# Performance work log

Measured on AMD Instinct MI355X. Metric: run time of the kernel, lower is better.

The kernel has to match this reference:

```python
import jax, jax.numpy as jnp
import numpy as np

T, B, E, H = 512, 64, 256, 256


def setup_inputs() -> dict:
    key = jax.random.key(0)
    ks = jax.random.split(key, 14)
    def p(k, shape, s=0.05):
        return jax.random.normal(k, shape, dtype=jnp.float32) * s
    return {
        "inputs": jax.random.normal(ks[0], (T, B, E), dtype=jnp.float32),
        # attention params (nn.Parameter torch.randn -> unit scale)
        "rot": jax.random.normal(ks[1], (E, E), dtype=jnp.float32),
        "ent": jax.random.normal(ks[2], (E, E), dtype=jnp.float32),
        # gate linears: stored as (in, out) so y = x @ W + b (same math as torch Linear)
        "Wf": p(ks[3], (E + H, H)), "bf": jnp.zeros((H,), jnp.float32),
        "Wi": p(ks[4], (E + H, H)), "bi": jnp.zeros((H,), jnp.float32),
        "Wu": p(ks[5], (E + H, H)), "bu": jnp.zeros((H,), jnp.float32),
        "Wo": p(ks[6], (E + H, H)), "bo": jnp.zeros((H,), jnp.float32),
        "Wc": p(ks[7], (E, H)),     "bc": jnp.zeros((H,), jnp.float32),
    }


def reference(inputs, rot, ent, Wf, bf, Wi, bi, Wu, bu, Wo, bo, Wc, bc):
    t, b, e = inputs.shape
    h = Wf.shape[1]
    # --- one-shot self-attention (ClassicalSelfAttention) ---
    inp = inputs.transpose(1, 0, 2)                       # [B,T,E]
    q = jnp.einsum('bte,ef->btf', inp, rot)
    k = jnp.einsum('bte,ef->btf', inp, ent)
    scores = jax.nn.softmax(jnp.einsum('btf,bsf->bts', q, k) / jnp.sqrt(jnp.float32(e)), axis=-1)
    context = jnp.einsum('bts,bse->bte', scores, inp).transpose(1, 0, 2)  # [T,B,E]
    # context projection is time-invariant -> precompute as one big GEMM
    ctx_proj = context @ Wc + bc                          # [T,B,H]
    # --- recurrent LSTM cell over time via scan ---
    def step(carry, xs):
        hx, cx = carry
        x, cp = xs
        combined = jnp.concatenate([x, hx + cp], axis=1)  # [B,E+H]
        f = jax.nn.sigmoid(combined @ Wf + bf)
        i = jax.nn.sigmoid(combined @ Wi + bi)
        g = jnp.tanh(combined @ Wu + bu)
        o = jax.nn.sigmoid(combined @ Wo + bo)
        cx = f * cx + i * g
        hx = o * jnp.tanh(cx)
        return (hx, cx), hx
    hx0 = jnp.zeros((b, h), inputs.dtype)
    cx0 = jnp.zeros((b, h), inputs.dtype)
    (hx, cx), outputs = jax.lax.scan(step, (hx0, cx0), (inputs, ctx_proj))
    return outputs, hx, cx
```

## Files before the change

kernel.cpp:

```cpp
#include <hip/hip_runtime.h>

#define T_ 512
#define B_ 64
#define E_ 256
#define H_ 256

typedef __attribute__((ext_vector_type(8))) short short8_t;
typedef __attribute__((ext_vector_type(4))) float floatx4;

__device__ __forceinline__ unsigned short f2bf(float f) {
  unsigned int u = __float_as_uint(f);
  u += 0x7FFFu + ((u >> 16) & 1u);
  return (unsigned short)(u >> 16);
}
__device__ __forceinline__ float bf2f(unsigned short s) {
  return __uint_as_float(((unsigned int)s) << 16);
}
__device__ __forceinline__ float fast_tanh(float x) {
  float e = __expf(-2.0f * x);
  return 2.0f / (1.0f + e) - 1.0f;
}

__global__ __launch_bounds__(256) void qk_kernel(
    const float* __restrict__ inp, const float* __restrict__ rot,
    const float* __restrict__ ent, float* __restrict__ qo, float* __restrict__ ko)
{
  __shared__ __align__(16) float As[16][136];
  __shared__ __align__(16) float B1[16][68];
  __shared__ __align__(16) float B2[16][68];
  const int tid = threadIdx.x;
  const int m0 = blockIdx.y * 128, n0 = blockIdx.x * 64;
  const int lk = tid & 15, lm = tid >> 4;
  const int ln = tid & 63, lkb = tid >> 6;
  const int tx = tid & 15, ty = tid >> 4;
  float acc1[8][4], acc2[8][4];
#pragma unroll
  for (int i = 0; i < 8; ++i)
#pragma unroll
    for (int j = 0; j < 4; ++j) { acc1[i][j] = 0.f; acc2[i][j] = 0.f; }

  for (int k0 = 0; k0 < 256; k0 += 16) {
    __syncthreads();
#pragma unroll
    for (int p = 0; p < 8; ++p) {
      int m = lm + p * 16;
      As[lk][m] = inp[(size_t)(m0 + m) * 256 + k0 + lk];
    }
#pragma unroll
    for (int p = 0; p < 4; ++p) {
      int kk = lkb + p * 4;
      B1[kk][ln] = rot[(size_t)(k0 + kk) * 256 + n0 + ln];
      B2[kk][ln] = ent[(size_t)(k0 + kk) * 256 + n0 + ln];
    }
    __syncthreads();
#pragma unroll
    for (int kk = 0; kk < 16; ++kk) {
      floatx4 a_lo = *(const floatx4*)&As[kk][ty * 8];
      floatx4 a_hi = *(const floatx4*)&As[kk][ty * 8 + 4];
      floatx4 b1v = *(const floatx4*)&B1[kk][tx * 4];
      floatx4 b2v = *(const floatx4*)&B2[kk][tx * 4];
#pragma unroll
      for (int i = 0; i < 4; ++i) {
        float alo = a_lo[i], ahi = a_hi[i];
#pragma unroll
        for (int j = 0; j < 4; ++j) {
          acc1[i][j]     += alo * b1v[j];
          acc1[i + 4][j] += ahi * b1v[j];
          acc2[i][j]     += alo * b2v[j];
          acc2[i + 4][j] += ahi * b2v[j];
        }
      }
    }
  }
#pragma unroll
  for (int i = 0; i < 8; ++i) {
    size_t row = (size_t)(m0 + ty * 8 + i);
    float4 v1 = make_float4(acc1[i][0], acc1[i][1], acc1[i][2], acc1[i][3]);
    float4 v2 = make_float4(acc2[i][0], acc2[i][1], acc2[i][2], acc2[i][3]);
    *(float4*)&qo[row * 256 + n0 + tx * 4] = v1;
    *(float4*)&ko[row * 256 + n0 + tx * 4] = v2;
  }
}

__global__ __launch_bounds__(256) void scores_kernel(
    const float* __restrict__ q, const float* __restrict__ k, float* __restrict__ S)
{
  __shared__ __align__(16) float As[16][136];
  __shared__ __align__(16) float Bs[16][136];
  const int tid = threadIdx.x;
  const int b = blockIdx.z;
  const int m0 = blockIdx.y * 128, n0 = blockIdx.x * 128;
  const int lk = tid & 15, lm = tid >> 4;
  const int tx = tid & 15, ty = tid >> 4;
  float acc[8][8];
#pragma unroll
  for (int i = 0; i < 8; ++i)
#pragma unroll
    for (int j = 0; j < 8; ++j) acc[i][j] = 0.f;

  const float* Ab = q + (size_t)b * 256;
  const float* Bb = k + (size_t)b * 256;
  for (int k0 = 0; k0 < 256; k0 += 16) {
    __syncthreads();
#pragma unroll
    for (int p = 0; p < 8; ++p) {
      int m = lm + p * 16;
      As[lk][m] = Ab[(size_t)(m0 + m) * 16384 + k0 + lk];
      Bs[lk][m] = Bb[(size_t)(n0 + m) * 16384 + k0 + lk];
    }
    __syncthreads();
#pragma unroll
    for (int kk = 0; kk < 16; ++kk) {
      floatx4 a_lo = *(const floatx4*)&As[kk][ty * 8];
      floatx4 a_hi = *(const floatx4*)&As[kk][ty * 8 + 4];
      floatx4 b_lo = *(const floatx4*)&Bs[kk][tx * 8];
      floatx4 b_hi = *(const floatx4*)&Bs[kk][tx * 8 + 4];
      float av[8], bv[8];
#pragma unroll
      for (int i = 0; i < 4; ++i) { av[i] = a_lo[i]; av[i + 4] = a_hi[i];
                                    bv[i] = b_lo[i]; bv[i + 4] = b_hi[i]; }
#pragma unroll
      for (int i = 0; i < 8; ++i)
#pragma unroll
        for (int j = 0; j < 8; ++j)
          acc[i][j] += av[i] * bv[j];
    }
  }
#pragma unroll
  for (int i = 0; i < 8; ++i) {
    size_t off = (size_t)b * 262144 + (size_t)(m0 + ty * 8 + i) * 512 + n0 + tx * 8;
    float4 v0 = make_float4(acc[i][0] * 0.0625f, acc[i][1] * 0.0625f,
                            acc[i][2] * 0.0625f, acc[i][3] * 0.0625f);
    float4 v1 = make_float4(acc[i][4] * 0.0625f, acc[i][5] * 0.0625f,
                            acc[i][6] * 0.0625f, acc[i][7] * 0.0625f);
    *(float4*)&S[off] = v0;
    *(float4*)&S[off + 4] = v1;
  }
}

__global__ __launch_bounds__(256) void softmax_kernel(float* __restrict__ S)
{
  float* p = S + (size_t)blockIdx.x * 512;
  const int tid = threadIdx.x;
  float x0 = p[tid], x1 = p[tid + 256];
  float m = fmaxf(x0, x1);
#pragma unroll
  for (int off = 32; off > 0; off >>= 1) m = fmaxf(m, __shfl_xor(m, off));
  __shared__ float red[8];
  const int wv = tid >> 6;
  if ((tid & 63) == 0) red[wv] = m;
  __syncthreads();
  m = fmaxf(fmaxf(red[0], red[1]), fmaxf(red[2], red[3]));
  float e0 = __expf(x0 - m);
  float e1 = __expf(x1 - m);
  float s = e0 + e1;
#pragma unroll
  for (int off = 32; off > 0; off >>= 1) s += __shfl_xor(s, off);
  if ((tid & 63) == 0) red[4 + wv] = s;
  __syncthreads();
  s = red[4] + red[5] + red[6] + red[7];
  float r = 1.0f / s;
  p[tid] = e0 * r;
  p[tid + 256] = e1 * r;
}

__global__ __launch_bounds__(256) void context_kernel(
    const float* __restrict__ P, const float* __restrict__ inp, float* __restrict__ ctx)
{
  __shared__ __align__(16) float As[16][136];
  __shared__ __align__(16) float Bs[16][136];
  const int tid = threadIdx.x;
  const int b = blockIdx.z;
  const int m0 = blockIdx.y * 128, e0 = blockIdx.x * 128;
  const int lk = tid & 15, lm = tid >> 4;
  const int tx = tid & 15, ty = tid >> 4;
  const int bk = tid >> 7, be = tid & 127;
  float acc[8][8];
#pragma unroll
  for (int i = 0; i < 8; ++i)
#pragma unroll
    for (int j = 0; j < 8; ++j) acc[i][j] = 0.f;

  const float* Ab = P + (size_t)b * 262144;
  for (int k0 = 0; k0 < 512; k0 += 16) {
    __syncthreads();
#pragma unroll
    for (int p = 0; p < 8; ++p) {
      int m = lm + p * 16;
      As[lk][m] = Ab[(size_t)(m0 + m) * 512 + k0 + lk];
    }
#pragma unroll
    for (int p = 0; p < 8; ++p) {
      int kk = bk + p * 2;
      Bs[kk][be] = inp[(size_t)(k0 + kk) * 16384 + b * 256 + e0 + be];
    }
    __syncthreads();
#pragma unroll
    for (int kk = 0; kk < 16; ++kk) {
      floatx4 a_lo = *(const floatx4*)&As[kk][ty * 8];
      floatx4 a_hi = *(const floatx4*)&As[kk][ty * 8 + 4];
      floatx4 b_lo = *(const floatx4*)&Bs[kk][tx * 8];
      floatx4 b_hi = *(const floatx4*)&Bs[kk][tx * 8 + 4];
      float av[8], bv[8];
#pragma unroll
      for (int i = 0; i < 4; ++i) { av[i] = a_lo[i]; av[i + 4] = a_hi[i];
                                    bv[i] = b_lo[i]; bv[i + 4] = b_hi[i]; }
#pragma unroll
      for (int i = 0; i < 8; ++i)
#pragma unroll
        for (int j = 0; j < 8; ++j)
          acc[i][j] += av[i] * bv[j];
    }
  }
#pragma unroll
  for (int i = 0; i < 8; ++i) {
    size_t off = (size_t)(m0 + ty * 8 + i) * 16384 + (size_t)b * 256 + e0 + tx * 8;
    float4 v0 = make_float4(acc[i][0], acc[i][1], acc[i][2], acc[i][3]);
    float4 v1 = make_float4(acc[i][4], acc[i][5], acc[i][6], acc[i][7]);
    *(float4*)&ctx[off] = v0;
    *(float4*)&ctx[off + 4] = v1;
  }
}

__global__ __launch_bounds__(256) void cp_kernel(
    const float* __restrict__ ctx, const float* __restrict__ Wc,
    const float* __restrict__ bc, float* __restrict__ cp)
{
  __shared__ __align__(16) float As[16][136];
  __shared__ __align__(16) float Bs[16][68];
  const int tid = threadIdx.x;
  const int m0 = blockIdx.y * 128, n0 = blockIdx.x * 64;
  const int lk = tid & 15, lm = tid >> 4;
  const int ln = tid & 63, lkb = tid >> 6;
  const int tx = tid & 15, ty = tid >> 4;
  float acc[8][4];
#pragma unroll
  for (int i = 0; i < 8; ++i)
#pragma unroll
    for (int j = 0; j < 4; ++j) acc[i][j] = 0.f;

  for (int k0 = 0; k0 < 256; k0 += 16) {
    __syncthreads();
#pragma unroll
    for (int p = 0; p < 8; ++p) {
      int m = lm + p * 16;
      As[lk][m] = ctx[(size_t)(m0 + m) * 256 + k0 + lk];
    }
#pragma unroll
    for (int p = 0; p < 4; ++p) {
      int kk = lkb + p * 4;
      Bs[kk][ln] = Wc[(size_t)(k0 + kk) * 256 + n0 + ln];
    }
    __syncthreads();
#pragma unroll
    for (int kk = 0; kk < 16; ++kk) {
      floatx4 a_lo = *(const floatx4*)&As[kk][ty * 8];
      floatx4 a_hi = *(const floatx4*)&As[kk][ty * 8 + 4];
      floatx4 bv = *(const floatx4*)&Bs[kk][tx * 4];
#pragma unroll
      for (int i = 0; i < 4; ++i) {
        float alo = a_lo[i], ahi = a_hi[i];
#pragma unroll
        for (int j = 0; j < 4; ++j) {
          acc[i][j]     += alo * bv[j];
          acc[i + 4][j] += ahi * bv[j];
        }
      }
    }
  }
  float b0 = bc[n0 + tx * 4 + 0], b1 = bc[n0 + tx * 4 + 1];
  float b2 = bc[n0 + tx * 4 + 2], b3 = bc[n0 + tx * 4 + 3];
#pragma unroll
  for (int i = 0; i < 8; ++i) {
    size_t row = (size_t)(m0 + ty * 8 + i);
    float4 v = make_float4(acc[i][0] + b0, acc[i][1] + b1, acc[i][2] + b2, acc[i][3] + b3);
    *(float4*)&cp[row * 256 + n0 + tx * 4] = v;
  }
}

__global__ __launch_bounds__(256) void pack_w(
    const float* __restrict__ Wf, const float* __restrict__ Wi,
    const float* __restrict__ Wu, const float* __restrict__ Wo,
    const float* __restrict__ bfv, const float* __restrict__ biv,
    const float* __restrict__ buv, const float* __restrict__ bov,
    unsigned short* __restrict__ Wt, float* __restrict__ bcat)
{
  const int n = blockIdx.x;
  const int g = n >> 8, h = n & 255;
  const float* W = (g == 0) ? Wf : (g == 1) ? Wi : (g == 2) ? Wu : Wo;
  const float* bb = (g == 0) ? bfv : (g == 1) ? biv : (g == 2) ? buv : bov;
  for (int k = threadIdx.x; k < 512; k += 256)
    Wt[(size_t)n * 512 + k] = f2bf(W[(size_t)k * 256 + h]);
  if (threadIdx.x == 0) bcat[n] = bb[h];
}

__global__ __launch_bounds__(256) void gemm_pre(
    const float* __restrict__ x, const float* __restrict__ cp,
    const unsigned short* __restrict__ Wt, const float* __restrict__ bcat,
    unsigned short* __restrict__ pre)
{
  __shared__ __align__(16) unsigned short As[64 * 40];
  __shared__ __align__(16) unsigned short Bs[64 * 40];
  const int tid = threadIdx.x;
  const int n0 = blockIdx.x * 64, m0 = blockIdx.y * 64;
  const int lane = tid & 63, wv = tid >> 6;
  const int lm = lane & 15, qd = lane >> 4;
  const int sr = tid >> 2, sk = (tid & 3) * 8;
  floatx4 acc[4] = {{0.f,0.f,0.f,0.f},{0.f,0.f,0.f,0.f},
                    {0.f,0.f,0.f,0.f},{0.f,0.f,0.f,0.f}};
  for (int k0 = 0; k0 < 512; k0 += 32) {
    const float* Asrc = (k0 < 256)
        ? (x  + (size_t)(m0 + sr) * 256 + k0 + sk)
        : (cp + (size_t)(m0 + sr) * 256 + (k0 - 256) + sk);
    float4 a0 = *(const float4*)Asrc;
    float4 a1 = *(const float4*)(Asrc + 4);
    short8_t av;
    av[0] = (short)f2bf(a0.x); av[1] = (short)f2bf(a0.y);
    av[2] = (short)f2bf(a0.z); av[3] = (short)f2bf(a0.w);
    av[4] = (short)f2bf(a1.x); av[5] = (short)f2bf(a1.y);
    av[6] = (short)f2bf(a1.z); av[7] = (short)f2bf(a1.w);
    short8_t bv = *(const short8_t*)&Wt[(size_t)(n0 + sr) * 512 + k0 + sk];
    *(short8_t*)&As[sr * 40 + sk] = av;
    *(short8_t*)&Bs[sr * 40 + sk] = bv;
    __syncthreads();
    short8_t af = *(const short8_t*)&As[(wv * 16 + lm) * 40 + qd * 8];
#pragma unroll
    for (int nt = 0; nt < 4; ++nt) {
      short8_t bf = *(const short8_t*)&Bs[(nt * 16 + lm) * 40 + qd * 8];
      acc[nt] = __builtin_amdgcn_mfma_f32_16x16x32_bf16(af, bf, acc[nt], 0, 0, 0);
    }
    __syncthreads();
  }
#pragma unroll
  for (int nt = 0; nt < 4; ++nt) {
    int col = n0 + nt * 16 + lm;
    float bb = bcat[col];
    int col2 = ((col & 255) << 2) | (col >> 8);
#pragma unroll
    for (int r = 0; r < 4; ++r) {
      int row = m0 + wv * 16 + qd * 4 + r;
      pre[(size_t)row * 1024 + col2] = f2bf(acc[nt][r] + bb);
    }
  }
}

__global__ __launch_bounds__(256, 1) void scan_kernel(
    const unsigned short* __restrict__ pre,
    const unsigned short* __restrict__ Wt,
    float* __restrict__ out, unsigned long long* __restrict__ hxT)
{
  __shared__ __align__(16) unsigned short hl[2][16 * 264];
  const int tid = threadIdx.x;
  const int bg = blockIdx.x >> 2;
  const int cg = blockIdx.x & 3;
  const int lane = tid & 63;
  const int w = tid >> 6;
  const int qd = lane >> 4;
  const int lh = lane & 15;

  {
    unsigned long long* z = (unsigned long long*)hl;
    for (int i = tid; i < 2112; i += 256) z[i] = 0ull;
  }

  short8_t wreg[4][8];
#pragma unroll
  for (int g = 0; g < 4; ++g)
#pragma unroll
    for (int kc = 0; kc < 8; ++kc)
      wreg[g][kc] = *(const short8_t*)&Wt[(size_t)(g * 256 + cg * 64 + w * 16 + lh) * 512
                                          + 256 + kc * 32 + qd * 8];

  const unsigned long long* pq = (const unsigned long long*)pre;
  const int orow0 = bg * 16 + qd * 4;
  const int hcol = cg * 64 + w * 16 + lh;
  unsigned long long pcur[4], pnext[4];
#pragma unroll
  for (int r = 0; r < 4; ++r)
    pcur[r] = pq[(size_t)(orow0 + r) * 256 + hcol];

  float cst[4] = {0.f, 0.f, 0.f, 0.f};
  const int cg1 = (cg + 1) & 3, cg2 = (cg + 2) & 3, cg3 = (cg + 3) & 3;
  const int prow = tid >> 4, pcolq = tid & 15;

  __syncthreads();

#pragma unroll 1
  for (int t = 0; t < 512; ++t) {
    unsigned long long* hlqR = (unsigned long long*)hl[t & 1];
    unsigned long long* hlqW = (unsigned long long*)hl[(t + 1) & 1];

    if (t > 0) {
      const unsigned long long* sbase = hxT + (size_t)((t - 1) * 4 + bg) * 1024;
      const unsigned long long* s0 = sbase + (size_t)cg1 * 256;
      const unsigned long long* s1 = sbase + (size_t)cg2 * 256;
      const unsigned long long* s2 = sbase + (size_t)cg3 * 256;
      unsigned long long d0, d1, d2;
      bool ok;
      do {
        d0 = __hip_atomic_load(&s0[tid], __ATOMIC_RELAXED, __HIP_MEMORY_SCOPE_AGENT);
        d1 = __hip_atomic_load(&s1[tid], __ATOMIC_RELAXED, __HIP_MEMORY_SCOPE_AGENT);
        d2 = __hip_atomic_load(&s2[tid], __ATOMIC_RELAXED, __HIP_MEMORY_SCOPE_AGENT);
        ok = ((unsigned int)d0 != 0xFFFFFFFFu) && ((unsigned int)(d0 >> 32) != 0xFFFFFFFFu)
          && ((unsigned int)d1 != 0xFFFFFFFFu) && ((unsigned int)(d1 >> 32) != 0xFFFFFFFFu)
          && ((unsigned int)d2 != 0xFFFFFFFFu) && ((unsigned int)(d2 >> 32) != 0xFFFFFFFFu);
      } while (!__all((int)ok));
      hlqR[prow * 66 + cg1 * 16 + pcolq] = d0;
      hlqR[prow * 66 + cg2 * 16 + pcolq] = d1;
      hlqR[prow * 66 + cg3 * 16 + pcolq] = d2;
    }

    if (t < 511) {
      size_t base = (size_t)((t + 1) * 64 + orow0) * 256 + hcol;
#pragma unroll
      for (int r = 0; r < 4; ++r)
        pnext[r] = pq[base + (size_t)r * 256];
    }

    __syncthreads();

    const unsigned short* hb = hl[t & 1];
    floatx4 acc[4] = {{0.f,0.f,0.f,0.f},{0.f,0.f,0.f,0.f},
                      {0.f,0.f,0.f,0.f},{0.f,0.f,0.f,0.f}};
#pragma unroll
    for (int kc = 0; kc < 8; ++kc) {
      short8_t av = *(const short8_t*)&hb[lh * 264 + kc * 32 + qd * 8];
#pragma unroll
      for (int g = 0; g < 4; ++g)
        acc[g] = __builtin_amdgcn_mfma_f32_16x16x32_bf16(av, wreg[g][kc], acc[g], 0, 0, 0);
    }

    float h[4];
#pragma unroll
    for (int r = 0; r < 4; ++r) {
      unsigned long long pv = pcur[r];
      float xf = acc[0][r] + bf2f((unsigned short)pv);
      float xi = acc[1][r] + bf2f((unsigned short)(pv >> 16));
      float xu = acc[2][r] + bf2f((unsigned short)(pv >> 32));
      float xo = acc[3][r] + bf2f((unsigned short)(pv >> 48));
      float fg = 1.0f / (1.0f + __expf(-xf));
      float ig = 1.0f / (1.0f + __expf(-xi));
      float gg = fast_tanh(xu);
      float og = 1.0f / (1.0f + __expf(-xo));
      float cc = fg * cst[r] + ig * gg;
      cst[r] = cc;
      h[r] = og * fast_tanh(cc);
    }

    float t0c, t1c, t2c, t3c;
    {
      float e0 = __shfl_xor(h[0], 1);
      float e1 = __shfl_xor(h[1], 1);
      float e2 = __shfl_xor(h[2], 1);
      float e3 = __shfl_xor(h[3], 1);
      bool odd = (lane & 1);
      float b0 = odd ? e1 : h[0];
      float b1 = odd ? h[1] : e0;
      float b2 = odd ? e3 : h[2];
      float b3 = odd ? h[3] : e2;
      float f0 = __shfl_xor(b0, 2);
      float f1 = __shfl_xor(b1, 2);
      float f2 = __shfl_xor(b2, 2);
      float f3 = __shfl_xor(b3, 2);
      bool hi = (lane & 2);
      t0c = hi ? f2 : b0;
      t1c = hi ? f3 : b1;
      t2c = hi ? b2 : f0;
      t3c = hi ? b3 : f1;
    }
    unsigned long long hp = (unsigned long long)f2bf(t0c)
        | ((unsigned long long)f2bf(t1c) << 16)
        | ((unsigned long long)f2bf(t2c) << 32)
        | ((unsigned long long)f2bf(t3c) << 48);
    const int orow = qd * 4 + (lane & 3);
    const int ocolq = w * 4 + (lh >> 2);

    __hip_atomic_store(&hxT[(size_t)((t * 4 + bg) * 4 + cg) * 256 + orow * 16 + ocolq],
                       hp, __ATOMIC_RELAXED, __HIP_MEMORY_SCOPE_AGENT);
    hlqW[orow * 66 + cg * 16 + ocolq] = hp;
    *(float4*)&out[(size_t)t * 16384 + (size_t)(bg * 16 + orow) * 256 + cg * 64 + ocolq * 4]
        = make_float4(t0c, t1c, t2c, t3c);

    if (t == 511) {
      const size_t hoff = (size_t)512 * 16384;
#pragma unroll
      for (int r = 0; r < 4; ++r) {
        out[hoff + (size_t)(orow0 + r) * 256 + hcol] = h[r];
        out[hoff + 16384 + (size_t)(orow0 + r) * 256 + hcol] = cst[r];
      }
    }
#pragma unroll
    for (int r = 0; r < 4; ++r) pcur[r] = pnext[r];
  }
}

extern "C" void kernel_launch(void* const* d_in, const int* in_sizes, int n_in,
                              void* d_out, int out_size, void* d_ws, size_t ws_size,
                              hipStream_t stream)
{
  const float* inputs = (const float*)d_in[0];
  const float* rot = (const float*)d_in[1];
  const float* ent = (const float*)d_in[2];
  const float* Wf = (const float*)d_in[3];
  const float* bf_ = (const float*)d_in[4];
  const float* Wi = (const float*)d_in[5];
  const float* bi_ = (const float*)d_in[6];
  const float* Wu = (const float*)d_in[7];
  const float* bu_ = (const float*)d_in[8];
  const float* Wo = (const float*)d_in[9];
  const float* bo_ = (const float*)d_in[10];
  const float* Wc = (const float*)d_in[11];
  const float* bc_ = (const float*)d_in[12];
  float* out = (float*)d_out;

  char* ws = (char*)d_ws;
  float* q  = (float*)(ws);
  float* kb = (float*)(ws + (size_t)32 * 1024 * 1024);
  float* S  = (float*)(ws + (size_t)64 * 1024 * 1024);
  unsigned short* pre = (unsigned short*)S;
  float* ctx = q;
  float* cp  = kb;
  unsigned short* Wcat = (unsigned short*)ws;
  float* bcat = (float*)(ws + (size_t)1048576);
  unsigned long long* hxT =
      (unsigned long long*)(ws + (size_t)2 * 1024 * 1024);

  qk_kernel<<<dim3(4, 256), 256, 0, stream>>>(inputs, rot, ent, q, kb);
  scores_kernel<<<dim3(4, 4, 64), 256, 0, stream>>>(q, kb, S);
  softmax_kernel<<<dim3(32768), 256, 0, stream>>>(S);
  context_kernel<<<dim3(2, 4, 64), 256, 0, stream>>>(S, inputs, ctx);
  cp_kernel<<<dim3(4, 256), 256, 0, stream>>>(ctx, Wc, bc_, cp);
  hipMemsetAsync(hxT, 0xFF, (size_t)16 * 1024 * 1024, stream);
  pack_w<<<dim3(1024), 256, 0, stream>>>(Wf, Wi, Wu, Wo, bf_, bi_, bu_, bo_,
                                         Wcat, bcat);
  gemm_pre<<<dim3(16, 512), 256, 0, stream>>>(inputs, cp, Wcat, bcat, pre);
  scan_kernel<<<dim3(16), 256, 0, stream>>>(pre, Wcat, out, hxT);
}
```

Baseline: 1.720 ms.

## Quantize recurrent weights to int8 and run each batch group in one block

The recurrent weights and hidden state are quantized to int8 with per-column scales, and the scan uses int8 MFMA. The weights are split between registers and 128KB of LDS. Each of the 4 blocks now owns a whole 16-row batch group across all hidden columns, so the cross-block atomic polling through global memory and the 16MB memset go away. The cost is lower precision, since h is quantized to 1/127 steps and the int8 weights carry error that can accumulate over 512 steps, plus only 4 CUs doing the serial work.

```diff
diff --git a/kernel.cpp b/kernel.cpp
--- a/kernel.cpp
+++ b/kernel.cpp
@@ -7,6 +7,7 @@
 
 typedef __attribute__((ext_vector_type(8))) short short8_t;
 typedef __attribute__((ext_vector_type(4))) float floatx4;
+typedef __attribute__((ext_vector_type(4))) int intx4;
 
 __device__ __forceinline__ unsigned short f2bf(float f) {
   unsigned int u = __float_as_uint(f);
@@ -283,15 +284,35 @@
     const float* __restrict__ Wu, const float* __restrict__ Wo,
     const float* __restrict__ bfv, const float* __restrict__ biv,
     const float* __restrict__ buv, const float* __restrict__ bov,
-    unsigned short* __restrict__ Wt, float* __restrict__ bcat)
+    unsigned short* __restrict__ Wt, float* __restrict__ bcat,
+    signed char* __restrict__ Wq, float* __restrict__ wscale)
 {
   const int n = blockIdx.x;
   const int g = n >> 8, h = n & 255;
   const float* W = (g == 0) ? Wf : (g == 1) ? Wi : (g == 2) ? Wu : Wo;
   const float* bb = (g == 0) ? bfv : (g == 1) ? biv : (g == 2) ? buv : bov;
-  for (int k = threadIdx.x; k < 512; k += 256)
+  const int tid = threadIdx.x;
+  for (int k = tid; k < 512; k += 256)
     Wt[(size_t)n * 512 + k] = f2bf(W[(size_t)k * 256 + h]);
-  if (threadIdx.x == 0) bcat[n] = bb[h];
+  if (tid == 0) bcat[n] = bb[h];
+
+  float v = W[(size_t)(256 + tid) * 256 + h];
+  float a = fabsf(v);
+#pragma unroll
+  for (int off = 32; off > 0; off >>= 1) a = fmaxf(a, __shfl_xor(a, off));
+  __shared__ float mx[4];
+  if ((tid & 63) == 0) mx[tid >> 6] = a;
+  __syncthreads();
+  float m = fmaxf(fmaxf(mx[0], mx[1]), fmaxf(mx[2], mx[3]));
+  float s = fmaxf(m, 1e-12f) * (1.0f / 127.0f);
+  int qv = (int)rintf(v / s);
+  qv = qv < -127 ? -127 : (qv > 127 ? 127 : qv);
+  const int w = h >> 5, hi = (h >> 4) & 1, lm = h & 15;
+  const int nt = g * 2 + hi;
+  const int kc = tid >> 6, qd = (tid >> 4) & 3, bb2 = tid & 15;
+  const int lane = qd * 16 + lm;
+  Wq[(size_t)(((w * 8 + nt) * 4 + kc)) * 1024 + lane * 16 + bb2] = (signed char)qv;
+  if (tid == 0) wscale[w * 128 + nt * 16 + lm] = s * (1.0f / 127.0f);
 }
 
 __global__ __launch_bounds__(256) void gemm_pre(
@@ -344,153 +365,116 @@
   }
 }
 
-__global__ __launch_bounds__(256, 1) void scan_kernel(
+__global__ __launch_bounds__(512, 2) void scan_kernel(
     const unsigned short* __restrict__ pre,
-    const unsigned short* __restrict__ Wt,
-    float* __restrict__ out, unsigned long long* __restrict__ hxT)
-{
-  __shared__ __align__(16) unsigned short hl[2][16 * 264];
-  const int tid = threadIdx.x;
-  const int bg = blockIdx.x >> 2;
-  const int cg = blockIdx.x & 3;
+    const signed char* __restrict__ Wq,
+    const float* __restrict__ wscale,
+    float* __restrict__ out)
+{
+  __shared__ __align__(16) signed char wlds[131072];
+  __shared__ __align__(16) signed char hq[2][16 * 272];
+  const int tid = threadIdx.x;
+  const int bg = blockIdx.x;
   const int lane = tid & 63;
   const int w = tid >> 6;
   const int qd = lane >> 4;
-  const int lh = lane & 15;
+  const int lm = lane & 15;
 
   {
-    unsigned long long* z = (unsigned long long*)hl;
-    for (int i = tid; i < 2112; i += 256) z[i] = 0ull;
-  }
-
-  short8_t wreg[4][8];
-#pragma unroll
-  for (int g = 0; g < 4; ++g)
-#pragma unroll
-    for (int kc = 0; kc < 8; ++kc)
-      wreg[g][kc] = *(const short8_t*)&Wt[(size_t)(g * 256 + cg * 64 + w * 16 + lh) * 512
-                                          + 256 + kc * 32 + qd * 8];
+    unsigned long long* z = (unsigned long long*)hq;
+    for (int i = tid; i < 1088; i += 512) z[i] = 0ull;
+  }
+
+  intx4 wreg[8][2];
+#pragma unroll
+  for (int nt = 0; nt < 8; ++nt) {
+#pragma unroll
+    for (int kc = 0; kc < 4; ++kc) {
+      intx4 v = *(const intx4*)&Wq[(size_t)(((w * 8 + nt) * 4 + kc)) * 1024 + lane * 16];
+      if (kc < 2) wreg[nt][kc] = v;
+      else *(intx4*)&wlds[w * 16384 + (nt * 2 + (kc - 2)) * 1024 + lane * 16] = v;
+    }
+  }
+  float ws[8];
+#pragma unroll
+  for (int nt = 0; nt < 8; ++nt) ws[nt] = wscale[w * 128 + nt * 16 + lm];
 
   const unsigned long long* pq = (const unsigned long long*)pre;
-  const int orow0 = bg * 16 + qd * 4;
-  const int hcol = cg * 64 + w * 16 + lh;
-  unsigned long long pcur[4], pnext[4];
-#pragma unroll
-  for (int r = 0; r < 4; ++r)
-    pcur[r] = pq[(size_t)(orow0 + r) * 256 + hcol];
-
-  float cst[4] = {0.f, 0.f, 0.f, 0.f};
-  const int cg1 = (cg + 1) & 3, cg2 = (cg + 2) & 3, cg3 = (cg + 3) & 3;
-  const int prow = tid >> 4, pcolq = tid & 15;
+  const int row0 = bg * 16 + qd * 4;
+  const int c0 = w * 32 + lm, c1 = c0 + 16;
+  unsigned long long pcur[2][4], pnext[2][4];
+#pragma unroll
+  for (int r = 0; r < 4; ++r) {
+    pcur[0][r] = pq[(size_t)(row0 + r) * 256 + c0];
+    pcur[1][r] = pq[(size_t)(row0 + r) * 256 + c1];
+  }
+  float cst[2][4] = {{0.f,0.f,0.f,0.f},{0.f,0.f,0.f,0.f}};
 
   __syncthreads();
 
 #pragma unroll 1
   for (int t = 0; t < 512; ++t) {
-    unsigned long long* hlqR = (unsigned long long*)hl[t & 1];
-    unsigned long long* hlqW = (unsigned long long*)hl[(t + 1) & 1];
-
-    if (t > 0) {
-      const unsigned long long* sbase = hxT + (size_t)((t - 1) * 4 + bg) * 1024;
-      const unsigned long long* s0 = sbase + (size_t)cg1 * 256;
-      const unsigned long long* s1 = sbase + (size_t)cg2 * 256;
-      const unsigned long long* s2 = sbase + (size_t)cg3 * 256;
-      unsigned long long d0, d1, d2;
-      bool ok;
-      do {
-        d0 = __hip_atomic_load(&s0[tid], __ATOMIC_RELAXED, __HIP_MEMORY_SCOPE_AGENT);
-        d1 = __hip_atomic_load(&s1[tid], __ATOMIC_RELAXED, __HIP_MEMORY_SCOPE_AGENT);
-        d2 = __hip_atomic_load(&s2[tid], __ATOMIC_RELAXED, __HIP_MEMORY_SCOPE_AGENT);
-        ok = ((unsigned int)d0 != 0xFFFFFFFFu) && ((unsigned int)(d0 >> 32) != 0xFFFFFFFFu)
-          && ((unsigned int)d1 != 0xFFFFFFFFu) && ((unsigned int)(d1 >> 32) != 0xFFFFFFFFu)
-          && ((unsigned int)d2 != 0xFFFFFFFFu) && ((unsigned int)(d2 >> 32) != 0xFFFFFFFFu);
-      } while (!__all((int)ok));
-      hlqR[prow * 66 + cg1 * 16 + pcolq] = d0;
-      hlqR[prow * 66 + cg2 * 16 + pcolq] = d1;
-      hlqR[prow * 66 + cg3 * 16 + pcolq] = d2;
-    }
+    const signed char* hR = hq[t & 1];
+    signed char* hW = hq[(t + 1) & 1];
 
     if (t < 511) {
-      size_t base = (size_t)((t + 1) * 64 + orow0) * 256 + hcol;
-#pragma unroll
-      for (int r = 0; r < 4; ++r)
-        pnext[r] = pq[base + (size_t)r * 256];
-    }
-
-    __syncthreads();
-
-    const unsigned short* hb = hl[t & 1];
-    floatx4 acc[4] = {{0.f,0.f,0.f,0.f},{0.f,0.f,0.f,0.f},
-                      {0.f,0.f,0.f,0.f},{0.f,0.f,0.f,0.f}};
-#pragma unroll
-    for (int kc = 0; kc < 8; ++kc) {
-      short8_t av = *(const short8_t*)&hb[lh * 264 + kc * 32 + qd * 8];
-#pragma unroll
-      for (int g = 0; g < 4; ++g)
-        acc[g] = __builtin_amdgcn_mfma_f32_16x16x32_bf16(av, wreg[g][kc], acc[g], 0, 0, 0);
-    }
-
-    float h[4];
+      size_t base = (size_t)((t + 1) * 64 + row0) * 256;
+#pragma unroll
+      for (int r = 0; r < 4; ++r) {
+        pnext[0][r] = pq[base + (size_t)r * 256 + c0];
+        pnext[1][r] = pq[base + (size_t)r * 256 + c1];
+      }
+    }
+
+    intx4 acc[8];
+#pragma unroll
+    for (int nt = 0; nt < 8; ++nt) acc[nt] = (intx4){0, 0, 0, 0};
+#pragma unroll
+    for (int kc = 0; kc < 4; ++kc) {
+      intx4 av = *(const intx4*)&hR[lm * 272 + kc * 64 + qd * 16];
+#pragma unroll
+      for (int nt = 0; nt < 8; ++nt) {
+        intx4 bv;
+        if (kc < 2) bv = wreg[nt][kc];
+        else bv = *(const intx4*)&wlds[w * 16384 + (nt * 2 + (kc - 2)) * 1024 + lane * 16];
+        acc[nt] = __builtin_amdgcn_mfma_i32_16x16x64_i8(av, bv, acc[nt], 0, 0, 0);
+      }
+    }
+
+#pragma unroll
+    for (int hi = 0; hi < 2; ++hi) {
+      const int col = hi ? c1 : c0;
+#pragma unroll
+      for (int r = 0; r < 4; ++r) {
+        unsigned long long pv = pcur[hi][r];
+        float xf = (float)acc[0 + hi][r] * ws[0 + hi] + bf2f((unsigned short)pv);
+        float xi = (float)acc[2 + hi][r] * ws[2 + hi] + bf2f((unsigned short)(pv >> 16));
+        float xu = (float)acc[4 + hi][r] * ws[4 + hi] + bf2f((unsigned short)(pv >> 32));
+        float xo = (float)acc[6 + hi][r] * ws[6 + hi] + bf2f((unsigned short)(pv >> 48));
+        float fg = 1.0f / (1.0f + __expf(-xf));
+        float ig = 1.0f / (1.0f + __expf(-xi));
+        float gg = fast_tanh(xu);
+        float og = 1.0f / (1.0f + __expf(-xo));
+        float cc = fg * cst[hi][r] + ig * gg;
+        cst[hi][r] = cc;
+        float hh = og * fast_tanh(cc);
+        int hv = (int)rintf(hh * 127.0f);
+        hv = hv < -127 ? -127 : (hv > 127 ? 127 : hv);
+        hW[(qd * 4 + r) * 272 + col] = (signed char)hv;
+        out[(size_t)t * 16384 + (size_t)(row0 + r) * 256 + col] = hh;
+        if (t == 511) {
+          const size_t hoff = (size_t)512 * 16384 + (size_t)(row0 + r) * 256 + col;
+          out[hoff] = hh;
+          out[hoff + 16384] = cc;
+        }
+      }
+    }
 #pragma unroll
     for (int r = 0; r < 4; ++r) {
-      unsigned long long pv = pcur[r];
-      float xf = acc[0][r] + bf2f((unsigned short)pv);
-      float xi = acc[1][r] + bf2f((unsigned short)(pv >> 16));
-      float xu = acc[2][r] + bf2f((unsigned short)(pv >> 32));
-      float xo = acc[3][r] + bf2f((unsigned short)(pv >> 48));
-      float fg = 1.0f / (1.0f + __expf(-xf));
-      float ig = 1.0f / (1.0f + __expf(-xi));
-      float gg = fast_tanh(xu);
-      float og = 1.0f / (1.0f + __expf(-xo));
-      float cc = fg * cst[r] + ig * gg;
-      cst[r] = cc;
-      h[r] = og * fast_tanh(cc);
-    }
-
-    float t0c, t1c, t2c, t3c;
-    {
-      float e0 = __shfl_xor(h[0], 1);
-      float e1 = __shfl_xor(h[1], 1);
-      float e2 = __shfl_xor(h[2], 1);
-      float e3 = __shfl_xor(h[3], 1);
-      bool odd = (lane & 1);
-      float b0 = odd ? e1 : h[0];
-      float b1 = odd ? h[1] : e0;
-      float b2 = odd ? e3 : h[2];
-      float b3 = odd ? h[3] : e2;
-      float f0 = __shfl_xor(b0, 2);
-      float f1 = __shfl_xor(b1, 2);
-      float f2 = __shfl_xor(b2, 2);
-      float f3 = __shfl_xor(b3, 2);
-      bool hi = (lane & 2);
-      t0c = hi ? f2 : b0;
-      t1c = hi ? f3 : b1;
-      t2c = hi ? b2 : f0;
-      t3c = hi ? b3 : f1;
-    }
-    unsigned long long hp = (unsigned long long)f2bf(t0c)
-        | ((unsigned long long)f2bf(t1c) << 16)
-        | ((unsigned long long)f2bf(t2c) << 32)
-        | ((unsigned long long)f2bf(t3c) << 48);
-    const int orow = qd * 4 + (lane & 3);
-    const int ocolq = w * 4 + (lh >> 2);
-
-    __hip_atomic_store(&hxT[(size_t)((t * 4 + bg) * 4 + cg) * 256 + orow * 16 + ocolq],
-                       hp, __ATOMIC_RELAXED, __HIP_MEMORY_SCOPE_AGENT);
-    hlqW[orow * 66 + cg * 16 + ocolq] = hp;
-    *(float4*)&out[(size_t)t * 16384 + (size_t)(bg * 16 + orow) * 256 + cg * 64 + ocolq * 4]
-        = make_float4(t0c, t1c, t2c, t3c);
-
-    if (t == 511) {
-      const size_t hoff = (size_t)512 * 16384;
-#pragma unroll
-      for (int r = 0; r < 4; ++r) {
-        out[hoff + (size_t)(orow0 + r) * 256 + hcol] = h[r];
-        out[hoff + 16384 + (size_t)(orow0 + r) * 256 + hcol] = cst[r];
-      }
-    }
-#pragma unroll
-    for (int r = 0; r < 4; ++r) pcur[r] = pnext[r];
+      pcur[0][r] = pnext[0][r];
+      pcur[1][r] = pnext[1][r];
+    }
+    __syncthreads();
   }
 }
 
@@ -522,17 +506,16 @@
   float* cp  = kb;
   unsigned short* Wcat = (unsigned short*)ws;
   float* bcat = (float*)(ws + (size_t)1048576);
-  unsigned long long* hxT =
-      (unsigned long long*)(ws + (size_t)2 * 1024 * 1024);
+  signed char* Wq = (signed char*)(ws + (size_t)2 * 1024 * 1024);
+  float* wscale = (float*)(ws + (size_t)2 * 1024 * 1024 + 262144);
 
   qk_kernel<<<dim3(4, 256), 256, 0, stream>>>(inputs, rot, ent, q, kb);
   scores_kernel<<<dim3(4, 4, 64), 256, 0, stream>>>(q, kb, S);
   softmax_kernel<<<dim3(32768), 256, 0, stream>>>(S);
   context_kernel<<<dim3(2, 4, 64), 256, 0, stream>>>(S, inputs, ctx);
   cp_kernel<<<dim3(4, 256), 256, 0, stream>>>(ctx, Wc, bc_, cp);
-  hipMemsetAsync(hxT, 0xFF, (size_t)16 * 1024 * 1024, stream);
   pack_w<<<dim3(1024), 256, 0, stream>>>(Wf, Wi, Wu, Wo, bf_, bi_, bu_, bo_,
-                                         Wcat, bcat);
+                                         Wcat, bcat, Wq, wscale);
   gemm_pre<<<dim3(16, 512), 256, 0, stream>>>(inputs, cp, Wcat, bcat, pre);
-  scan_kernel<<<dim3(16), 256, 0, stream>>>(pre, Wcat, out, hxT);
-}
+  scan_kernel<<<dim3(4), 512, 0, stream>>>(pre, Wq, wscale, out);
+}
```

After: 2.460 ms. +43.0%, slower.

## Fold context projection Wc into LSTM gate weights, drop cp GEMM

Applied to the files above, without the earlier changes.

Removes the separate ctx@Wc GEMM by precomputing Wc·W_h for each gate (plus bc·W_h folded into the bias), so gemm_pre reads the context directly. This eliminates a 32768x256x256 fp32 GEMM and the write and read of the cp buffer. In exchange it adds a small fold kernel, and the combined weights are rounded to bf16, which may change numerical error slightly. Workspace offsets are moved so the new buffers do not collide.

```diff
diff --git a/kernel.cpp b/kernel.cpp
--- a/kernel.cpp
+++ b/kernel.cpp
@@ -222,62 +222,6 @@
   }
 }
 
-__global__ __launch_bounds__(256) void cp_kernel(
-    const float* __restrict__ ctx, const float* __restrict__ Wc,
-    const float* __restrict__ bc, float* __restrict__ cp)
-{
-  __shared__ __align__(16) float As[16][136];
-  __shared__ __align__(16) float Bs[16][68];
-  const int tid = threadIdx.x;
-  const int m0 = blockIdx.y * 128, n0 = blockIdx.x * 64;
-  const int lk = tid & 15, lm = tid >> 4;
-  const int ln = tid & 63, lkb = tid >> 6;
-  const int tx = tid & 15, ty = tid >> 4;
-  float acc[8][4];
-#pragma unroll
-  for (int i = 0; i < 8; ++i)
-#pragma unroll
-    for (int j = 0; j < 4; ++j) acc[i][j] = 0.f;
-
-  for (int k0 = 0; k0 < 256; k0 += 16) {
-    __syncthreads();
-#pragma unroll
-    for (int p = 0; p < 8; ++p) {
-      int m = lm + p * 16;
-      As[lk][m] = ctx[(size_t)(m0 + m) * 256 + k0 + lk];
-    }
-#pragma unroll
-    for (int p = 0; p < 4; ++p) {
-      int kk = lkb + p * 4;
-      Bs[kk][ln] = Wc[(size_t)(k0 + kk) * 256 + n0 + ln];
-    }
-    __syncthreads();
-#pragma unroll
-    for (int kk = 0; kk < 16; ++kk) {
-      floatx4 a_lo = *(const floatx4*)&As[kk][ty * 8];
-      floatx4 a_hi = *(const floatx4*)&As[kk][ty * 8 + 4];
-      floatx4 bv = *(const floatx4*)&Bs[kk][tx * 4];
-#pragma unroll
-      for (int i = 0; i < 4; ++i) {
-        float alo = a_lo[i], ahi = a_hi[i];
-#pragma unroll
-        for (int j = 0; j < 4; ++j) {
-          acc[i][j]     += alo * bv[j];
-          acc[i + 4][j] += ahi * bv[j];
-        }
-      }
-    }
-  }
-  float b0 = bc[n0 + tx * 4 + 0], b1 = bc[n0 + tx * 4 + 1];
-  float b2 = bc[n0 + tx * 4 + 2], b3 = bc[n0 + tx * 4 + 3];
-#pragma unroll
-  for (int i = 0; i < 8; ++i) {
-    size_t row = (size_t)(m0 + ty * 8 + i);
-    float4 v = make_float4(acc[i][0] + b0, acc[i][1] + b1, acc[i][2] + b2, acc[i][3] + b3);
-    *(float4*)&cp[row * 256 + n0 + tx * 4] = v;
-  }
-}
-
 __global__ __launch_bounds__(256) void pack_w(
     const float* __restrict__ Wf, const float* __restrict__ Wi,
     const float* __restrict__ Wu, const float* __restrict__ Wo,
@@ -294,9 +238,44 @@
   if (threadIdx.x == 0) bcat[n] = bb[h];
 }
 
+__global__ __launch_bounds__(256) void fold_wc(
+    const float* __restrict__ Wf, const float* __restrict__ Wi,
+    const float* __restrict__ Wu, const float* __restrict__ Wo,
+    const float* __restrict__ bfv, const float* __restrict__ biv,
+    const float* __restrict__ buv, const float* __restrict__ bov,
+    const float* __restrict__ Wc, const float* __restrict__ bc,
+    unsigned short* __restrict__ Wt2, float* __restrict__ bcat2)
+{
+  const int n = blockIdx.x;
+  const int g = n >> 8, h = n & 255;
+  const float* W = (g == 0) ? Wf : (g == 1) ? Wi : (g == 2) ? Wu : Wo;
+  const float* bb = (g == 0) ? bfv : (g == 1) ? biv : (g == 2) ? buv : bov;
+  const int tid = threadIdx.x;
+  __shared__ float wl[256];
+  __shared__ float red[4];
+
+  Wt2[(size_t)n * 512 + tid] = f2bf(W[(size_t)tid * 256 + h]);
+  float wv = W[(size_t)(256 + tid) * 256 + h];
+  wl[tid] = wv;
+  __syncthreads();
+
+  float s = 0.f;
+#pragma unroll 8
+  for (int j = 0; j < 256; ++j)
+    s += Wc[(size_t)tid * 256 + j] * wl[j];
+  Wt2[(size_t)n * 512 + 256 + tid] = f2bf(s);
+
+  float p = bc[tid] * wv;
+#pragma unroll
+  for (int off = 32; off > 0; off >>= 1) p += __shfl_xor(p, off);
+  if ((tid & 63) == 0) red[tid >> 6] = p;
+  __syncthreads();
+  if (tid == 0) bcat2[n] = bb[h] + red[0] + red[1] + red[2] + red[3];
+}
+
 __global__ __launch_bounds__(256) void gemm_pre(
-    const float* __restrict__ x, const float* __restrict__ cp,
-    const unsigned short* __restrict__ Wt, const float* __restrict__ bcat,
+    const float* __restrict__ x, const float* __restrict__ ctx,
+    const unsigned short* __restrict__ Wt2, const float* __restrict__ bcat2,
     unsigned short* __restrict__ pre)
 {
   __shared__ __align__(16) unsigned short As[64 * 40];
@@ -310,8 +289,8 @@
                     {0.f,0.f,0.f,0.f},{0.f,0.f,0.f,0.f}};
   for (int k0 = 0; k0 < 512; k0 += 32) {
     const float* Asrc = (k0 < 256)
-        ? (x  + (size_t)(m0 + sr) * 256 + k0 + sk)
-        : (cp + (size_t)(m0 + sr) * 256 + (k0 - 256) + sk);
+        ? (x   + (size_t)(m0 + sr) * 256 + k0 + sk)
+        : (ctx + (size_t)(m0 + sr) * 256 + (k0 - 256) + sk);
     float4 a0 = *(const float4*)Asrc;
     float4 a1 = *(const float4*)(Asrc + 4);
     short8_t av;
@@ -319,7 +298,7 @@
     av[2] = (short)f2bf(a0.z); av[3] = (short)f2bf(a0.w);
     av[4] = (short)f2bf(a1.x); av[5] = (short)f2bf(a1.y);
     av[6] = (short)f2bf(a1.z); av[7] = (short)f2bf(a1.w);
-    short8_t bv = *(const short8_t*)&Wt[(size_t)(n0 + sr) * 512 + k0 + sk];
+    short8_t bv = *(const short8_t*)&Wt2[(size_t)(n0 + sr) * 512 + k0 + sk];
     *(short8_t*)&As[sr * 40 + sk] = av;
     *(short8_t*)&Bs[sr * 40 + sk] = bv;
     __syncthreads();
@@ -334,7 +313,7 @@
 #pragma unroll
   for (int nt = 0; nt < 4; ++nt) {
     int col = n0 + nt * 16 + lm;
-    float bb = bcat[col];
+    float bb = bcat2[col];
     int col2 = ((col & 255) << 2) | (col >> 8);
 #pragma unroll
     for (int r = 0; r < 4; ++r) {
@@ -519,20 +498,22 @@
   float* S  = (float*)(ws + (size_t)64 * 1024 * 1024);
   unsigned short* pre = (unsigned short*)S;
   float* ctx = q;
-  float* cp  = kb;
-  unsigned short* Wcat = (unsigned short*)ws;
-  float* bcat = (float*)(ws + (size_t)1048576);
+  unsigned short* Wcat  = (unsigned short*)(ws + (size_t)32 * 1024 * 1024);
+  float* bcat           = (float*)(ws + (size_t)33 * 1024 * 1024);
+  unsigned short* Wcat2 = (unsigned short*)(ws + (size_t)34 * 1024 * 1024);
+  float* bcat2          = (float*)(ws + (size_t)35 * 1024 * 1024);
   unsigned long long* hxT =
-      (unsigned long long*)(ws + (size_t)2 * 1024 * 1024);
+      (unsigned long long*)(ws + (size_t)36 * 1024 * 1024);
 
   qk_kernel<<<dim3(4, 256), 256, 0, stream>>>(inputs, rot, ent, q, kb);
   scores_kernel<<<dim3(4, 4, 64), 256, 0, stream>>>(q, kb, S);
   softmax_kernel<<<dim3(32768), 256, 0, stream>>>(S);
   context_kernel<<<dim3(2, 4, 64), 256, 0, stream>>>(S, inputs, ctx);
-  cp_kernel<<<dim3(4, 256), 256, 0, stream>>>(ctx, Wc, bc_, cp);
   hipMemsetAsync(hxT, 0xFF, (size_t)16 * 1024 * 1024, stream);
   pack_w<<<dim3(1024), 256, 0, stream>>>(Wf, Wi, Wu, Wo, bf_, bi_, bu_, bo_,
                                          Wcat, bcat);
-  gemm_pre<<<dim3(16, 512), 256, 0, stream>>>(inputs, cp, Wcat, bcat, pre);
+  fold_wc<<<dim3(1024), 256, 0, stream>>>(Wf, Wi, Wu, Wo, bf_, bi_, bu_, bo_,
+                                          Wc, bc_, Wcat2, bcat2);
+  gemm_pre<<<dim3(16, 512), 256, 0, stream>>>(inputs, ctx, Wcat2, bcat2, pre);
   scan_kernel<<<dim3(16), 256, 0, stream>>>(pre, Wcat, out, hxT);
 }
```

After: 1.678 ms. 2.4% less time.
